# Kernel tuning notes

Hardware: AMD Instinct MI355X
Metric: run time of the kernel (lower is better)

The kernel has to match this reference:

```python
import jax, jax.numpy as jnp
import numpy as np

WINDOW_SIZE = 11
SIGMA = 1.5
CHANNEL = 3


def _gaussian_window(window_size, sigma, channel):
    x = np.arange(window_size, dtype=np.float32)
    g = np.exp(-((x - window_size // 2) ** 2) / (2.0 * sigma ** 2))
    g = g / g.sum()
    w2d = np.outer(g, g).astype(np.float32)  # (ws, ws)
    # depthwise kernel: (C, 1, ws, ws) in OIHW with feature_group_count=C
    return jnp.asarray(np.broadcast_to(w2d, (channel, 1, window_size, window_size)).copy())


def _dwconv(x, w, pad):
    # x: (N, C, H, W), w: (C, 1, kh, kw), depthwise 'same' conv
    return jax.lax.conv_general_dilated(
        x, w, window_strides=(1, 1), padding=[(pad, pad), (pad, pad)],
        dimension_numbers=("NCHW", "OIHW", "NCHW"),
        feature_group_count=x.shape[1])


def setup_inputs() -> dict:
    key = jax.random.key(0)
    k1, k2 = jax.random.split(key)
    img1 = jax.random.uniform(k1, (32, 3, 512, 512), dtype=jnp.float32)
    img2 = jax.random.uniform(k2, (32, 3, 512, 512), dtype=jnp.float32)
    window = _gaussian_window(WINDOW_SIZE, SIGMA, CHANNEL)
    return {"img1": img1, "img2": img2, "window": window}


def reference(img1, img2, window):
    pad = WINDOW_SIZE // 2
    mu1 = _dwconv(img1, window, pad)
    mu2 = _dwconv(img2, window, pad)
    mu1_sq = mu1 * mu1
    mu2_sq = mu2 * mu2
    mu1_mu2 = mu1 * mu2
    sigma1_sq = _dwconv(img1 * img1, window, pad) - mu1_sq
    sigma2_sq = _dwconv(img2 * img2, window, pad) - mu2_sq
    sigma12 = _dwconv(img1 * img2, window, pad) - mu1_mu2

    C1 = 0.01 ** 2
    C2 = 0.03 ** 2
    C3 = C2 / 2.0

    a1 = jnp.abs(sigma1_sq)
    a2 = jnp.abs(sigma2_sq)
    s1 = jnp.sqrt(a1)
    s2 = jnp.sqrt(a2)

    L = (2.0 * mu1_mu2 + C1) / (mu1_sq + mu2_sq + C1)
    C = (2.0 * s1 * s2 + C2) / (a1 + a2 + C2)
    S = (sigma12 + C3) / (s1 * s2 + C3)

    return (L.mean(), C.mean(), S.mean())
```

## Files before the change

### kernel.cpp

```cpp
#include <hip/hip_runtime.h>
#include <math.h>

#define IMG 512
#define PLANES 96
#define XS_W 54
#define NXS 10
#define YS_H 64
#define NYS 8
#define WPB 4
#define NSLOT 32
#define ACC_STRIDE 16
#define INV_NPIX (1.0 / 25165824.0)


__global__ void ssim_init(double* __restrict__ acc, float* __restrict__ gwp,
                          const float* __restrict__ win) {
    int i = threadIdx.x;
    if (i < NSLOT * ACC_STRIDE) acc[i] = 0.0;
    if (i < 11) gwp[i] = sqrtf(win[i * 12]);
}

template<int P>
__device__ __forceinline__ void row_step(
    int T, int y0, bool col_ok,
    const float* __restrict__ p1, const float* __restrict__ p2,
    float& x1, float& x2, const int (&si)[11], const float* __restrict__ g,
    float (&A)[5][11], bool out_ok, float& sL, float& sC, float& sS)
{
    const int t = T + P;
    const int gy_next = y0 - 4 + t;
    float nx1 = 0.f, nx2 = 0.f;
    if (col_ok && (unsigned)gy_next < IMG) {
        int off = gy_next * IMG;
        nx1 = p1[off];
        nx2 = p2[off];
    }
    float a[11], b[11];
    #pragma unroll
    for (int j = 0; j < 11; ++j) {
        if (j == 5) { a[j] = x1; b[j] = x2; }
        else {
            a[j] = __int_as_float(__builtin_amdgcn_ds_bpermute(si[j], __float_as_int(x1)));
            b[j] = __int_as_float(__builtin_amdgcn_ds_bpermute(si[j], __float_as_int(x2)));
        }
    }
    float H1 = 0.f, H2 = 0.f, H11 = 0.f, H22 = 0.f, H12 = 0.f;
    #pragma unroll
    for (int j = 0; j < 11; ++j) {
        float w = g[j];
        float t1 = w * a[j], t2 = w * b[j];
        H1 += t1; H2 += t2;
        H11 = fmaf(t1, a[j], H11);
        H22 = fmaf(t2, b[j], H22);
        H12 = fmaf(t1, b[j], H12);
    }
    #pragma unroll
    for (int j = 0; j < 11; ++j) {
        const int s = (P + j + 1) % 11;
        float w = g[10 - j];
        A[0][s] = fmaf(w, H1,  A[0][s]);
        A[1][s] = fmaf(w, H2,  A[1][s]);
        A[2][s] = fmaf(w, H11, A[2][s]);
        A[3][s] = fmaf(w, H22, A[3][s]);
        A[4][s] = fmaf(w, H12, A[4][s]);
    }
    const int es = (P + 1) % 11;
    if (t >= 10 && t <= 73) {
        float mu1 = A[0][es], mu2 = A[1][es];
        float x11 = A[2][es], x22 = A[3][es], x12 = A[4][es];
        float mu1s = mu1 * mu1, mu2s = mu2 * mu2, mu12 = mu1 * mu2;
        float v1 = x11 - mu1s, v2 = x22 - mu2s, v12 = x12 - mu12;
        float a1 = fabsf(v1), a2 = fabsf(v2);
        float q12 = sqrtf(a1 * a2);
        const float C1 = 1e-4f, C2 = 9e-4f, C3 = 4.5e-4f;
        float eL = __fdividef(2.f * mu12 + C1, mu1s + mu2s + C1);
        float eC = __fdividef(2.f * q12 + C2, a1 + a2 + C2);
        float eS = __fdividef(v12 + C3, q12 + C3);
        if (out_ok) { sL += eL; sC += eC; sS += eS; }
    }
    #pragma unroll
    for (int q = 0; q < 5; ++q) A[q][es] = 0.f;
    x1 = nx1; x2 = nx2;
}

__global__ __launch_bounds__(256, 4) void ssim_main(
    const float* __restrict__ img1, const float* __restrict__ img2,
    const float* __restrict__ gwp, double* __restrict__ acc)
{
    const int lane = threadIdx.x & 63;
    const int wid  = blockIdx.x * WPB + (threadIdx.x >> 6);
    const int plane = wid / (NXS * NYS);
    const int rem   = wid % (NXS * NYS);
    const int ys = rem / NXS, xs = rem % NXS;
    const int x0 = xs * XS_W;
    const int y0 = ys * YS_H;
    const int col = x0 - 5 + lane;
    const bool col_ok = (unsigned)col < IMG;
    const bool out_ok = (lane >= 5) && (lane <= 58) && col_ok;

    const float* g = gwp;

    int si[11];
    #pragma unroll
    for (int j = 0; j < 11; ++j) si[j] = (lane + j - 5) << 2;

    const float* p1 = img1 + (size_t)plane * (IMG * IMG) + col;
    const float* p2 = img2 + (size_t)plane * (IMG * IMG) + col;

    float x1 = 0.f, x2 = 0.f;
    {
        int gy = y0 - 5;
        if (col_ok && (unsigned)gy < IMG) { x1 = p1[gy * IMG]; x2 = p2[gy * IMG]; }
    }

    float A[5][11];
    #pragma unroll
    for (int q = 0; q < 5; ++q)
        #pragma unroll
        for (int s = 0; s < 11; ++s) A[q][s] = 0.f;

    float sL = 0.f, sC = 0.f, sS = 0.f;

    #pragma unroll 1
    for (int T = 0; T < 66; T += 11) {
        row_step<0>(T, y0, col_ok, p1, p2, x1, x2, si, g, A, out_ok, sL, sC, sS);
        row_step<1>(T, y0, col_ok, p1, p2, x1, x2, si, g, A, out_ok, sL, sC, sS);
        row_step<2>(T, y0, col_ok, p1, p2, x1, x2, si, g, A, out_ok, sL, sC, sS);
        row_step<3>(T, y0, col_ok, p1, p2, x1, x2, si, g, A, out_ok, sL, sC, sS);
        row_step<4>(T, y0, col_ok, p1, p2, x1, x2, si, g, A, out_ok, sL, sC, sS);
        row_step<5>(T, y0, col_ok, p1, p2, x1, x2, si, g, A, out_ok, sL, sC, sS);
        row_step<6>(T, y0, col_ok, p1, p2, x1, x2, si, g, A, out_ok, sL, sC, sS);
        row_step<7>(T, y0, col_ok, p1, p2, x1, x2, si, g, A, out_ok, sL, sC, sS);
        row_step<8>(T, y0, col_ok, p1, p2, x1, x2, si, g, A, out_ok, sL, sC, sS);
        row_step<9>(T, y0, col_ok, p1, p2, x1, x2, si, g, A, out_ok, sL, sC, sS);
        row_step<10>(T, y0, col_ok, p1, p2, x1, x2, si, g, A, out_ok, sL, sC, sS);
    }
    row_step<0>(66, y0, col_ok, p1, p2, x1, x2, si, g, A, out_ok, sL, sC, sS);
    row_step<1>(66, y0, col_ok, p1, p2, x1, x2, si, g, A, out_ok, sL, sC, sS);
    row_step<2>(66, y0, col_ok, p1, p2, x1, x2, si, g, A, out_ok, sL, sC, sS);
    row_step<3>(66, y0, col_ok, p1, p2, x1, x2, si, g, A, out_ok, sL, sC, sS);
    row_step<4>(66, y0, col_ok, p1, p2, x1, x2, si, g, A, out_ok, sL, sC, sS);
    row_step<5>(66, y0, col_ok, p1, p2, x1, x2, si, g, A, out_ok, sL, sC, sS);
    row_step<6>(66, y0, col_ok, p1, p2, x1, x2, si, g, A, out_ok, sL, sC, sS);
    row_step<7>(66, y0, col_ok, p1, p2, x1, x2, si, g, A, out_ok, sL, sC, sS);

    #pragma unroll
    for (int off = 32; off > 0; off >>= 1) {
        sL += __shfl_down(sL, off, 64);
        sC += __shfl_down(sC, off, 64);
        sS += __shfl_down(sS, off, 64);
    }
    if (lane == 0) {
        double* slot = acc + (size_t)(wid & (NSLOT - 1)) * ACC_STRIDE;
        atomicAdd(slot + 0, (double)sL);
        atomicAdd(slot + 1, (double)sC);
        atomicAdd(slot + 2, (double)sS);
    }
}

__global__ void ssim_fin(const double* __restrict__ acc, float* __restrict__ out) {
    int i = threadIdx.x;
    if (i < 3) {
        double s = 0.0;
        for (int k = 0; k < NSLOT; ++k) s += acc[k * ACC_STRIDE + i];
        out[i] = (float)(s * INV_NPIX);
    }
}

extern "C" void kernel_launch(void* const* d_in, const int* in_sizes, int n_in,
                              void* d_out, int out_size, void* d_ws, size_t ws_size,
                              hipStream_t stream) {
    const float* img1 = (const float*)d_in[0];
    const float* img2 = (const float*)d_in[1];
    const float* win  = (const float*)d_in[2];
    float* out = (float*)d_out;
    double* acc = (double*)d_ws;
    float* gwp = (float*)((char*)d_ws + NSLOT * ACC_STRIDE * sizeof(double));

    ssim_init<<<1, 512, 0, stream>>>(acc, gwp, win);
    ssim_main<<<(PLANES * NXS * NYS) / WPB, 64 * WPB, 0, stream>>>(img1, img2, gwp, acc);
    ssim_fin<<<1, 64, 0, stream>>>(acc, out);
}
```

Baseline: 330.7 us.

## Replace LDS bpermute lane shifts with DPP wave shifts and prefetch rows deeper

The horizontal 11-tap neighbour gathers are rebuilt from chains of DPP whole-wave shift-by-one ops instead of 20 ds_bpermute calls per row, which takes traffic off the LDS path. Row loads are now prefetched two rows ahead, using clamped addresses and a select instead of a branch. Gaussian weights are computed per wave and kept uniform through readfirstlane. The init kernel is replaced by a memset. The DPP chains add serial dependency latency, the shift direction relies on the window being symmetric, and DPP wave-shift support depends on the target ISA.

```diff
diff --git a/kernel.cpp b/kernel.cpp
--- a/kernel.cpp
+++ b/kernel.cpp
@@ -12,38 +12,38 @@
 #define ACC_STRIDE 16
 #define INV_NPIX (1.0 / 25165824.0)
 
-
-__global__ void ssim_init(double* __restrict__ acc, float* __restrict__ gwp,
-                          const float* __restrict__ win) {
-    int i = threadIdx.x;
-    if (i < NSLOT * ACC_STRIDE) acc[i] = 0.0;
-    if (i < 11) gwp[i] = sqrtf(win[i * 12]);
+__device__ __forceinline__ float wshr1(float v) {
+    return __int_as_float(__builtin_amdgcn_update_dpp(0, __float_as_int(v), 0x138, 0xF, 0xF, true));
+}
+__device__ __forceinline__ float wshl1(float v) {
+    return __int_as_float(__builtin_amdgcn_update_dpp(0, __float_as_int(v), 0x130, 0xF, 0xF, true));
 }
 
 template<int P>
 __device__ __forceinline__ void row_step(
-    int T, int y0, bool col_ok,
+    int T, int y0, bool col_ok, int colc,
     const float* __restrict__ p1, const float* __restrict__ p2,
-    float& x1, float& x2, const int (&si)[11], const float* __restrict__ g,
-    float (&A)[5][11], bool out_ok, float& sL, float& sC, float& sS)
+    float& x1, float& x2, float& y1, float& y2,
+    const float (&g)[11], float (&A)[5][11],
+    bool out_ok, float& sL, float& sC, float& sS)
 {
     const int t = T + P;
-    const int gy_next = y0 - 4 + t;
-    float nx1 = 0.f, nx2 = 0.f;
-    if (col_ok && (unsigned)gy_next < IMG) {
-        int off = gy_next * IMG;
-        nx1 = p1[off];
-        nx2 = p2[off];
+    float f1 = 0.f, f2 = 0.f;
+    {
+        const int gy = y0 - 3 + t;
+        if ((unsigned)gy < IMG) {
+            float l1 = (p1 + gy * IMG)[colc];
+            float l2 = (p2 + gy * IMG)[colc];
+            f1 = col_ok ? l1 : 0.f;
+            f2 = col_ok ? l2 : 0.f;
+        }
     }
     float a[11], b[11];
-    #pragma unroll
-    for (int j = 0; j < 11; ++j) {
-        if (j == 5) { a[j] = x1; b[j] = x2; }
-        else {
-            a[j] = __int_as_float(__builtin_amdgcn_ds_bpermute(si[j], __float_as_int(x1)));
-            b[j] = __int_as_float(__builtin_amdgcn_ds_bpermute(si[j], __float_as_int(x2)));
-        }
-    }
+    a[5] = x1; b[5] = x2;
+    a[6] = wshr1(a[5]);  a[7] = wshr1(a[6]);  a[8] = wshr1(a[7]);  a[9] = wshr1(a[8]);  a[10] = wshr1(a[9]);
+    a[4] = wshl1(a[5]);  a[3] = wshl1(a[4]);  a[2] = wshl1(a[3]);  a[1] = wshl1(a[2]);  a[0]  = wshl1(a[1]);
+    b[6] = wshr1(b[5]);  b[7] = wshr1(b[6]);  b[8] = wshr1(b[7]);  b[9] = wshr1(b[8]);  b[10] = wshr1(b[9]);
+    b[4] = wshl1(b[5]);  b[3] = wshl1(b[4]);  b[2] = wshl1(b[3]);  b[1] = wshl1(b[2]);  b[0]  = wshl1(b[1]);
     float H1 = 0.f, H2 = 0.f, H11 = 0.f, H22 = 0.f, H12 = 0.f;
     #pragma unroll
     for (int j = 0; j < 11; ++j) {
@@ -65,7 +65,7 @@
         A[4][s] = fmaf(w, H12, A[4][s]);
     }
     const int es = (P + 1) % 11;
-    if (t >= 10 && t <= 73) {
+    if (t >= 10) {
         float mu1 = A[0][es], mu2 = A[1][es];
         float x11 = A[2][es], x22 = A[3][es], x12 = A[4][es];
         float mu1s = mu1 * mu1, mu2s = mu2 * mu2, mu12 = mu1 * mu2;
@@ -80,15 +80,15 @@
     }
     #pragma unroll
     for (int q = 0; q < 5; ++q) A[q][es] = 0.f;
-    x1 = nx1; x2 = nx2;
+    x1 = y1; x2 = y2; y1 = f1; y2 = f2;
 }
 
 __global__ __launch_bounds__(256, 4) void ssim_main(
     const float* __restrict__ img1, const float* __restrict__ img2,
-    const float* __restrict__ gwp, double* __restrict__ acc)
+    const float* __restrict__ win, double* __restrict__ acc)
 {
     const int lane = threadIdx.x & 63;
-    const int wid  = blockIdx.x * WPB + (threadIdx.x >> 6);
+    const int wid  = __builtin_amdgcn_readfirstlane(blockIdx.x * WPB + (threadIdx.x >> 6));
     const int plane = wid / (NXS * NYS);
     const int rem   = wid % (NXS * NYS);
     const int ys = rem / NXS, xs = rem % NXS;
@@ -96,21 +96,31 @@
     const int y0 = ys * YS_H;
     const int col = x0 - 5 + lane;
     const bool col_ok = (unsigned)col < IMG;
+    const int colc = min(max(col, 0), IMG - 1);
     const bool out_ok = (lane >= 5) && (lane <= 58) && col_ok;
 
-    const float* g = gwp;
+    float g[11];
+    #pragma unroll
+    for (int j = 0; j < 11; ++j)
+        g[j] = __int_as_float(__builtin_amdgcn_readfirstlane(__float_as_int(sqrtf(win[j * 12]))));
 
-    int si[11];
-    #pragma unroll
-    for (int j = 0; j < 11; ++j) si[j] = (lane + j - 5) << 2;
+    const float* p1 = img1 + (size_t)plane * (IMG * IMG);
+    const float* p2 = img2 + (size_t)plane * (IMG * IMG);
 
-    const float* p1 = img1 + (size_t)plane * (IMG * IMG) + col;
-    const float* p2 = img2 + (size_t)plane * (IMG * IMG) + col;
-
-    float x1 = 0.f, x2 = 0.f;
+    float x1 = 0.f, x2 = 0.f, y1 = 0.f, y2 = 0.f;
     {
         int gy = y0 - 5;
-        if (col_ok && (unsigned)gy < IMG) { x1 = p1[gy * IMG]; x2 = p2[gy * IMG]; }
+        if ((unsigned)gy < IMG) {
+            float l1 = (p1 + gy * IMG)[colc], l2 = (p2 + gy * IMG)[colc];
+            x1 = col_ok ? l1 : 0.f; x2 = col_ok ? l2 : 0.f;
+        }
+    }
+    {
+        int gy = y0 - 4;
+        if ((unsigned)gy < IMG) {
+            float l1 = (p1 + gy * IMG)[colc], l2 = (p2 + gy * IMG)[colc];
+            y1 = col_ok ? l1 : 0.f; y2 = col_ok ? l2 : 0.f;
+        }
     }
 
     float A[5][11];
@@ -123,26 +133,26 @@
 
     #pragma unroll 1
     for (int T = 0; T < 66; T += 11) {
-        row_step<0>(T, y0, col_ok, p1, p2, x1, x2, si, g, A, out_ok, sL, sC, sS);
-        row_step<1>(T, y0, col_ok, p1, p2, x1, x2, si, g, A, out_ok, sL, sC, sS);
-        row_step<2>(T, y0, col_ok, p1, p2, x1, x2, si, g, A, out_ok, sL, sC, sS);
-        row_step<3>(T, y0, col_ok, p1, p2, x1, x2, si, g, A, out_ok, sL, sC, sS);
-        row_step<4>(T, y0, col_ok, p1, p2, x1, x2, si, g, A, out_ok, sL, sC, sS);
-        row_step<5>(T, y0, col_ok, p1, p2, x1, x2, si, g, A, out_ok, sL, sC, sS);
-        row_step<6>(T, y0, col_ok, p1, p2, x1, x2, si, g, A, out_ok, sL, sC, sS);
-        row_step<7>(T, y0, col_ok, p1, p2, x1, x2, si, g, A, out_ok, sL, sC, sS);
-        row_step<8>(T, y0, col_ok, p1, p2, x1, x2, si, g, A, out_ok, sL, sC, sS);
-        row_step<9>(T, y0, col_ok, p1, p2, x1, x2, si, g, A, out_ok, sL, sC, sS);
-        row_step<10>(T, y0, col_ok, p1, p2, x1, x2, si, g, A, out_ok, sL, sC, sS);
+        row_step<0>(T, y0, col_ok, colc, p1, p2, x1, x2, y1, y2, g, A, out_ok, sL, sC, sS);
+        row_step<1>(T, y0, col_ok, colc, p1, p2, x1, x2, y1, y2, g, A, out_ok, sL, sC, sS);
+        row_step<2>(T, y0, col_ok, colc, p1, p2, x1, x2, y1, y2, g, A, out_ok, sL, sC, sS);
+        row_step<3>(T, y0, col_ok, colc, p1, p2, x1, x2, y1, y2, g, A, out_ok, sL, sC, sS);
+        row_step<4>(T, y0, col_ok, colc, p1, p2, x1, x2, y1, y2, g, A, out_ok, sL, sC, sS);
+        row_step<5>(T, y0, col_ok, colc, p1, p2, x1, x2, y1, y2, g, A, out_ok, sL, sC, sS);
+        row_step<6>(T, y0, col_ok, colc, p1, p2, x1, x2, y1, y2, g, A, out_ok, sL, sC, sS);
+        row_step<7>(T, y0, col_ok, colc, p1, p2, x1, x2, y1, y2, g, A, out_ok, sL, sC, sS);
+        row_step<8>(T, y0, col_ok, colc, p1, p2, x1, x2, y1, y2, g, A, out_ok, sL, sC, sS);
+        row_step<9>(T, y0, col_ok, colc, p1, p2, x1, x2, y1, y2, g, A, out_ok, sL, sC, sS);
+        row_step<10>(T, y0, col_ok, colc, p1, p2, x1, x2, y1, y2, g, A, out_ok, sL, sC, sS);
     }
-    row_step<0>(66, y0, col_ok, p1, p2, x1, x2, si, g, A, out_ok, sL, sC, sS);
-    row_step<1>(66, y0, col_ok, p1, p2, x1, x2, si, g, A, out_ok, sL, sC, sS);
-    row_step<2>(66, y0, col_ok, p1, p2, x1, x2, si, g, A, out_ok, sL, sC, sS);
-    row_step<3>(66, y0, col_ok, p1, p2, x1, x2, si, g, A, out_ok, sL, sC, sS);
-    row_step<4>(66, y0, col_ok, p1, p2, x1, x2, si, g, A, out_ok, sL, sC, sS);
-    row_step<5>(66, y0, col_ok, p1, p2, x1, x2, si, g, A, out_ok, sL, sC, sS);
-    row_step<6>(66, y0, col_ok, p1, p2, x1, x2, si, g, A, out_ok, sL, sC, sS);
-    row_step<7>(66, y0, col_ok, p1, p2, x1, x2, si, g, A, out_ok, sL, sC, sS);
+    row_step<0>(66, y0, col_ok, colc, p1, p2, x1, x2, y1, y2, g, A, out_ok, sL, sC, sS);
+    row_step<1>(66, y0, col_ok, colc, p1, p2, x1, x2, y1, y2, g, A, out_ok, sL, sC, sS);
+    row_step<2>(66, y0, col_ok, colc, p1, p2, x1, x2, y1, y2, g, A, out_ok, sL, sC, sS);
+    row_step<3>(66, y0, col_ok, colc, p1, p2, x1, x2, y1, y2, g, A, out_ok, sL, sC, sS);
+    row_step<4>(66, y0, col_ok, colc, p1, p2, x1, x2, y1, y2, g, A, out_ok, sL, sC, sS);
+    row_step<5>(66, y0, col_ok, colc, p1, p2, x1, x2, y1, y2, g, A, out_ok, sL, sC, sS);
+    row_step<6>(66, y0, col_ok, colc, p1, p2, x1, x2, y1, y2, g, A, out_ok, sL, sC, sS);
+    row_step<7>(66, y0, col_ok, colc, p1, p2, x1, x2, y1, y2, g, A, out_ok, sL, sC, sS);
 
     #pragma unroll
     for (int off = 32; off > 0; off >>= 1) {
@@ -175,9 +185,8 @@
     const float* win  = (const float*)d_in[2];
     float* out = (float*)d_out;
     double* acc = (double*)d_ws;
-    float* gwp = (float*)((char*)d_ws + NSLOT * ACC_STRIDE * sizeof(double));
 
-    ssim_init<<<1, 512, 0, stream>>>(acc, gwp, win);
-    ssim_main<<<(PLANES * NXS * NYS) / WPB, 64 * WPB, 0, stream>>>(img1, img2, gwp, acc);
+    hipMemsetAsync(d_ws, 0, NSLOT * ACC_STRIDE * sizeof(double), stream);
+    ssim_main<<<(PLANES * NXS * NYS) / WPB, 64 * WPB, 0, stream>>>(img1, img2, win, acc);
     ssim_fin<<<1, 64, 0, stream>>>(acc, out);
 }
```

Measured after the change: 363.6 us. 9.9% more time.
